# Kernel optimization log

Hardware: AMD Instinct MI355X
Metric: run time of the kernel (lower is better)

The kernel has to match this reference:

```python
import jax, jax.numpy as jnp
import numpy as np

EOS = 1          # endToken[0]
T = 50           # maxDecodingTime (hard-coded in module)
B, S = 64, 128   # batch, src_len
E_ENC = 1024     # enc_hidden_size (== dec_hidden_size, required by outNN)
H = 1024         # dec_hidden_size
EMB = 512        # embed_size
V = 32000        # output vocab


def setup_inputs() -> dict:
    key = jax.random.key(0)
    ks = jax.random.split(key, 10)
    def p(k, shape, fan_in):
        return jax.random.normal(k, shape, jnp.float32) / np.float32(np.sqrt(fan_in))
    return {
        'dec_initial_state': jax.random.normal(ks[0], (2, 1, B, H), jnp.float32),
        'enc_hiddens': jax.random.normal(ks[1], (B, S, E_ENC), jnp.float32),
        'enc_len': jax.random.randint(ks[2], (B,), 1, S + 1),
        'tgt': jax.random.randint(ks[3], (B, T), 0, V),  # unused in eval mode (training=False)
        'W_ih': p(ks[4], (4 * H, EMB), EMB),      # LSTM input weights (i,f,g,o)
        'W_hh': p(ks[5], (4 * H, H), H),          # LSTM hidden weights
        'b_lstm': jnp.zeros((4 * H,), jnp.float32),
        'W_attproj': p(ks[6], (H, E_ENC), E_ENC), # att_projection (no bias)
        'W_out': p(ks[7], (EMB, 2 * E_ENC), 2 * E_ENC),  # outNN (no bias)
        'W_vocab': p(ks[8], (V, EMB), EMB),       # vocab_projection (no bias)
        'emb_table': p(ks[9], (V, EMB), 1.0),     # seqEmb
    }


def reference(dec_initial_state, enc_hiddens, enc_len, tgt, W_ih, W_hh, b_lstm,
              W_attproj, W_out, W_vocab, emb_table):
    # eval mode: tgt unused, dropout is identity
    h0 = dec_initial_state[0, 0]  # [B,H]
    c0 = dec_initial_state[1, 0]  # [B,H]
    keys = jnp.einsum('bse,he->bsh', enc_hiddens, W_attproj)          # att keys [B,S,H]
    mask = jnp.arange(S)[None, :] < enc_len[:, None]                  # sent mask [B,S]
    NEG = jnp.float32(-1e9)
    prev0 = jnp.zeros((B, EMB), jnp.float32)
    tl0 = jnp.zeros((B,), jnp.int32)
    fl0 = jnp.zeros((B,), bool)

    def step(carry, t):
        h, c, prev, tl, fl = carry
        # LSTM cell
        gates = prev @ W_ih.T + h @ W_hh.T + b_lstm                   # [B,4H]
        i, f, g, o = jnp.split(gates, 4, axis=1)
        c = jax.nn.sigmoid(f) * c + jax.nn.sigmoid(i) * jnp.tanh(g)
        h = jax.nn.sigmoid(o) * jnp.tanh(c)
        # dot attention over encoder states
        scores = jnp.einsum('bsh,bh->bs', keys, h)
        alpha = jax.nn.softmax(jnp.where(mask, scores, NEG), axis=1)
        c_t = jnp.einsum('bs,bse->be', alpha, enc_hiddens)            # [B,E_ENC]
        dec = jnp.concatenate([h, c_t], axis=1) @ W_out.T             # [B,EMB]
        sym = jnp.argmax(dec @ W_vocab.T, axis=1)                     # greedy symbol
        prev = emb_table[sym]
        is_eos = sym == EOS
        tl = jnp.where(is_eos, t + 1, tl)
        fl = fl | is_eos
        return (h, c, prev, tl, fl), (dec, is_eos)

    (_, _, _, tl, _), (preds, eos_hist) = jax.lax.scan(
        step, (h0, c0, prev0, tl0, fl0), jnp.arange(T))
    tl = jnp.where(~eos_hist[-1], T, tl)       # torch: tgt_len[~ixEOS] = decoding_time
    preds = preds.transpose(1, 0, 2)           # [B,T,EMB]
    logP = jax.nn.log_softmax(preds @ W_vocab.T, axis=2)  # [B,T,V]
    return logP, tl
```

## Files before the change

kernel.cpp:

```cpp
#include <hip/hip_runtime.h>
#include <math.h>

#define BB  64
#define SS  128
#define HH  1024
#define EE  1024
#define EMBD 512
#define VV  32000
#define TT  50

#define OFF_H     0
#define OFF_C     65536
#define OFF_PREV  131072
#define OFF_HC    163840
#define OFF_GPART 294912
#define OFF_DPART 1867776
#define OFF_DEC   2129920
#define OFF_QPART 2162688
#define OFF_TVAL  2424832
#define OFF_TIDX  2456832
#define OFF_SYM   2488832
#define OFF_TL    2488896
#define OFF_KEYS  2488960
#define WS_NEED_KEYS ((size_t)(OFF_KEYS + 8388608) * 4)

template<bool BT>
__device__ __forceinline__ void gemm_tile(const float* __restrict__ A, int lda,
                                          const float* __restrict__ B, int ldb,
                                          float* __restrict__ C, size_t ldc, int K)
{
    __shared__ __attribute__((aligned(16))) float As[32][68];
    __shared__ __attribute__((aligned(16))) float Bs[32][68];
    int tid = threadIdx.x;
    int tx = tid & 15, ty = tid >> 4;
    float acc[4][4] = {};
    int lr = tid >> 2;
    int lk = (tid & 3) << 3;
    int bk = tid >> 3;
    int bn = (tid & 7) << 3;

    for (int kc = 0; kc < K; kc += 32) {
        float4 a0 = *(const float4*)(A + (size_t)lr * lda + kc + lk);
        float4 a1 = *(const float4*)(A + (size_t)lr * lda + kc + lk + 4);
        As[lk+0][lr] = a0.x; As[lk+1][lr] = a0.y; As[lk+2][lr] = a0.z; As[lk+3][lr] = a0.w;
        As[lk+4][lr] = a1.x; As[lk+5][lr] = a1.y; As[lk+6][lr] = a1.z; As[lk+7][lr] = a1.w;
        if (BT) {
            float4 b0 = *(const float4*)(B + (size_t)lr * ldb + kc + lk);
            float4 b1 = *(const float4*)(B + (size_t)lr * ldb + kc + lk + 4);
            Bs[lk+0][lr] = b0.x; Bs[lk+1][lr] = b0.y; Bs[lk+2][lr] = b0.z; Bs[lk+3][lr] = b0.w;
            Bs[lk+4][lr] = b1.x; Bs[lk+5][lr] = b1.y; Bs[lk+6][lr] = b1.z; Bs[lk+7][lr] = b1.w;
        } else {
            float4 b0 = *(const float4*)(B + (size_t)(kc + bk) * ldb + bn);
            float4 b1 = *(const float4*)(B + (size_t)(kc + bk) * ldb + bn + 4);
            *(float4*)&Bs[bk][bn]     = b0;
            *(float4*)&Bs[bk][bn + 4] = b1;
        }
        __syncthreads();
        #pragma unroll 8
        for (int k = 0; k < 32; ++k) {
            float4 av = *(const float4*)&As[k][ty << 2];
            float4 bv = *(const float4*)&Bs[k][tx << 2];
            float am[4] = {av.x, av.y, av.z, av.w};
            float bm[4] = {bv.x, bv.y, bv.z, bv.w};
            #pragma unroll
            for (int i = 0; i < 4; ++i)
                #pragma unroll
                for (int j = 0; j < 4; ++j)
                    acc[i][j] = fmaf(am[i], bm[j], acc[i][j]);
        }
        __syncthreads();
    }
    #pragma unroll
    for (int i = 0; i < 4; ++i) {
        float4 w = make_float4(acc[i][0], acc[i][1], acc[i][2], acc[i][3]);
        *(float4*)(C + (size_t)((ty << 2) + i) * ldc + (tx << 2)) = w;
    }
}

__global__ __launch_bounds__(256) void k_gemm_bt(const float* __restrict__ A, int lda,
                                                 const float* __restrict__ B, int ldb,
                                                 float* __restrict__ C, long long ldc,
                                                 int KC, long long partStride)
{
    int n0 = blockIdx.x << 6;
    int k0 = blockIdx.y * KC;
    gemm_tile<true>(A + k0, lda, B + (size_t)n0 * ldb + k0, ldb,
                    C + (size_t)blockIdx.y * partStride + n0, (size_t)ldc, KC);
}

__global__ __launch_bounds__(256) void k_gemm_bn(const float* __restrict__ A, int lda,
                                                 const float* __restrict__ B, int ldb,
                                                 float* __restrict__ C, long long ldc,
                                                 int KC, long long partStride)
{
    int n0 = blockIdx.x << 6;
    int k0 = blockIdx.y * KC;
    gemm_tile<false>(A + k0, lda, B + (size_t)k0 * ldb + n0, ldb,
                     C + (size_t)blockIdx.y * partStride + n0, (size_t)ldc, KC);
}

__global__ __launch_bounds__(256) void k_keys(const float* __restrict__ enc,
                                              const float* __restrict__ Wap,
                                              float* __restrict__ keys)
{
    int n0 = blockIdx.x << 6;
    int m0 = blockIdx.y << 6;
    gemm_tile<true>(enc + (size_t)m0 * EE, EE, Wap + (size_t)n0 * EE, EE,
                    keys + (size_t)m0 * HH + n0, (size_t)HH, EE);
}

__global__ __launch_bounds__(256) void k_gates(const float* __restrict__ prev,
                                               const float* __restrict__ h,
                                               const float* __restrict__ Wih,
                                               const float* __restrict__ Whh,
                                               float* __restrict__ part)
{
    int n0 = blockIdx.x << 6;
    int ks = blockIdx.y;
    const float* A; const float* Bp; int lda, ldb;
    if (ks < 2) { A = prev + ks * 256;      lda = EMBD; Bp = Wih + (size_t)n0 * EMBD + ks * 256;       ldb = EMBD; }
    else        { A = h + (ks - 2) * 256;   lda = HH;   Bp = Whh + (size_t)n0 * HH + (ks - 2) * 256;   ldb = HH;   }
    gemm_tile<true>(A, lda, Bp, ldb, part + (size_t)ks * 262144 + n0, 4096, 256);
}

__global__ void k_lstm(const float* __restrict__ part, const float* __restrict__ bias,
                       float* __restrict__ h, float* __restrict__ c, float* __restrict__ hc)
{
    int idx = blockIdx.x * 256 + threadIdx.x;
    int b = idx >> 10, j = idx & 1023;
    size_t base = (size_t)b * 4096;
    #define GATE(col) (part[base + (col)] + part[base + (col) + 262144] + part[base + (col) + 524288] \
                     + part[base + (col) + 786432] + part[base + (col) + 1048576] + part[base + (col) + 1310720] \
                     + bias[(col)])
    float gi = GATE(j);
    float gf = GATE(j + 1024);
    float gg = GATE(j + 2048);
    float go = GATE(j + 3072);
    #undef GATE
    float si = 1.f / (1.f + expf(-gi));
    float sf = 1.f / (1.f + expf(-gf));
    float so = 1.f / (1.f + expf(-go));
    float cn = sf * c[idx] + si * tanhf(gg);
    float hn = so * tanhf(cn);
    c[idx] = cn;
    h[idx] = hn;
    hc[(size_t)b * 2048 + j] = hn;
}

__global__ __launch_bounds__(1024) void k_attn(const float* __restrict__ keys,
                                               const float* __restrict__ enc,
                                               const int* __restrict__ enc_len,
                                               const float* __restrict__ h,
                                               float* __restrict__ hc)
{
    __shared__ float hs[1024];
    __shared__ float sc[128];
    __shared__ float4 red[3][256];
    int b = blockIdx.x, tid = threadIdx.x;
    hs[tid] = h[(size_t)b * 1024 + tid];
    __syncthreads();
    int lane = tid & 63, w = tid >> 6;
    const float* kb = keys + (size_t)b * SS * HH;
    for (int s = w; s < 128; s += 16) {
        const float* kr = kb + (size_t)s * 1024;
        float acc = 0.f;
        #pragma unroll
        for (int i = 0; i < 16; ++i) acc = fmaf(kr[i * 64 + lane], hs[i * 64 + lane], acc);
        #pragma unroll
        for (int off = 32; off; off >>= 1) acc += __shfl_xor(acc, off, 64);
        if (lane == 0) sc[s] = acc;
    }
    __syncthreads();
    int len = enc_len[b];
    if (tid < 64) {
        float a  = (tid < len)      ? sc[tid]      : -1e9f;
        float a2 = (tid + 64 < len) ? sc[tid + 64] : -1e9f;
        float m = fmaxf(a, a2);
        #pragma unroll
        for (int off = 32; off; off >>= 1) m = fmaxf(m, __shfl_xor(m, off, 64));
        float ea = expf(a - m), ea2 = expf(a2 - m);
        float ssum = ea + ea2;
        #pragma unroll
        for (int off = 32; off; off >>= 1) ssum += __shfl_xor(ssum, off, 64);
        sc[tid] = ea / ssum; sc[tid + 64] = ea2 / ssum;
    }
    __syncthreads();
    int g = tid >> 8, t2 = tid & 255;
    const float* eb = enc + (size_t)b * SS * EE;
    float4 a4 = make_float4(0.f, 0.f, 0.f, 0.f);
    for (int s = g * 32; s < g * 32 + 32; ++s) {
        float al = sc[s];
        float4 e = *(const float4*)(eb + (size_t)s * 1024 + t2 * 4);
        a4.x = fmaf(al, e.x, a4.x); a4.y = fmaf(al, e.y, a4.y);
        a4.z = fmaf(al, e.z, a4.z); a4.w = fmaf(al, e.w, a4.w);
    }
    if (g) red[g - 1][t2] = a4;
    __syncthreads();
    if (g == 0) {
        float4 r1 = red[0][t2], r2 = red[1][t2], r3 = red[2][t2];
        a4.x += r1.x + r2.x + r3.x; a4.y += r1.y + r2.y + r3.y;
        a4.z += r1.z + r2.z + r3.z; a4.w += r1.w + r2.w + r3.w;
        *(float4*)(hc + (size_t)b * 2048 + 1024 + t2 * 4) = a4;
    }
}

__global__ __launch_bounds__(256) void k_attn_fb(const float* __restrict__ qpart,
                                                 const float* __restrict__ enc,
                                                 const int* __restrict__ enc_len,
                                                 float* __restrict__ hc)
{
    __shared__ float qs[1024];
    __shared__ float sc[128];
    int b = blockIdx.x, tid = threadIdx.x;
    for (int e = tid; e < 1024; e += 256) {
        size_t o = (size_t)b * 1024 + e;
        qs[e] = qpart[o] + qpart[o + 65536] + qpart[o + 131072] + qpart[o + 196608];
    }
    __syncthreads();
    int lane = tid & 63, w = tid >> 6;
    const float* eb = enc + (size_t)b * SS * EE;
    for (int s = w; s < 128; s += 4) {
        const float* er = eb + (size_t)s * 1024;
        float acc = 0.f;
        #pragma unroll
        for (int i = 0; i < 16; ++i) acc = fmaf(er[i * 64 + lane], qs[i * 64 + lane], acc);
        #pragma unroll
        for (int off = 32; off; off >>= 1) acc += __shfl_xor(acc, off, 64);
        if (lane == 0) sc[s] = acc;
    }
    __syncthreads();
    int len = enc_len[b];
    if (tid < 64) {
        float a  = (tid < len)      ? sc[tid]      : -1e9f;
        float a2 = (tid + 64 < len) ? sc[tid + 64] : -1e9f;
        float m = fmaxf(a, a2);
        #pragma unroll
        for (int off = 32; off; off >>= 1) m = fmaxf(m, __shfl_xor(m, off, 64));
        float ea = expf(a - m), ea2 = expf(a2 - m);
        float ssum = ea + ea2;
        #pragma unroll
        for (int off = 32; off; off >>= 1) ssum += __shfl_xor(ssum, off, 64);
        sc[tid] = ea / ssum; sc[tid + 64] = ea2 / ssum;
    }
    __syncthreads();
    float acc[4] = {0.f, 0.f, 0.f, 0.f};
    for (int s = 0; s < 128; ++s) {
        float al = sc[s];
        const float* er = eb + (size_t)s * 1024;
        #pragma unroll
        for (int j = 0; j < 4; ++j) acc[j] = fmaf(al, er[tid + j * 256], acc[j]);
    }
    #pragma unroll
    for (int j = 0; j < 4; ++j) hc[(size_t)b * 2048 + 1024 + tid + j * 256] = acc[j];
}

__global__ void k_reduce_dec(const float* __restrict__ part, float* __restrict__ dec)
{
    int i = blockIdx.x * 256 + threadIdx.x;
    float s = 0.f;
    #pragma unroll
    for (int p = 0; p < 8; ++p) s += part[p * 32768 + i];
    dec[i] = s;
}

__global__ __launch_bounds__(256) void k_vocab(const float* __restrict__ A,
                                               const float* __restrict__ B,
                                               float* __restrict__ out, int t,
                                               float* __restrict__ tval, int* __restrict__ tidx)
{
    __shared__ __attribute__((aligned(16))) float As[32][68];
    __shared__ __attribute__((aligned(16))) float Bs[32][68];
    int n0 = blockIdx.x << 6;
    const float* Bp = B + (size_t)n0 * EMBD;
    int tid = threadIdx.x;
    int tx = tid & 15, ty = tid >> 4;
    float acc[4][4] = {};
    int lr = tid >> 2;
    int lk = (tid & 3) << 3;

    for (int kc = 0; kc < EMBD; kc += 32) {
        float4 a0 = *(const float4*)(A + (size_t)lr * EMBD + kc + lk);
        float4 a1 = *(const float4*)(A + (size_t)lr * EMBD + kc + lk + 4);
        As[lk+0][lr] = a0.x; As[lk+1][lr] = a0.y; As[lk+2][lr] = a0.z; As[lk+3][lr] = a0.w;
        As[lk+4][lr] = a1.x; As[lk+5][lr] = a1.y; As[lk+6][lr] = a1.z; As[lk+7][lr] = a1.w;
        float4 b0 = *(const float4*)(Bp + (size_t)lr * EMBD + kc + lk);
        float4 b1 = *(const float4*)(Bp + (size_t)lr * EMBD + kc + lk + 4);
        Bs[lk+0][lr] = b0.x; Bs[lk+1][lr] = b0.y; Bs[lk+2][lr] = b0.z; Bs[lk+3][lr] = b0.w;
        Bs[lk+4][lr] = b1.x; Bs[lk+5][lr] = b1.y; Bs[lk+6][lr] = b1.z; Bs[lk+7][lr] = b1.w;
        __syncthreads();
        #pragma unroll 8
        for (int k = 0; k < 32; ++k) {
            float4 av = *(const float4*)&As[k][ty << 2];
            float4 bv = *(const float4*)&Bs[k][tx << 2];
            float am[4] = {av.x, av.y, av.z, av.w};
            float bm[4] = {bv.x, bv.y, bv.z, bv.w};
            #pragma unroll
            for (int i = 0; i < 4; ++i)
                #pragma unroll
                for (int j = 0; j < 4; ++j)
                    acc[i][j] = fmaf(am[i], bm[j], acc[i][j]);
        }
        __syncthreads();
    }
    size_t ldc = (size_t)TT * VV;
    float* Cb = out + (size_t)t * VV + n0;
    #pragma unroll
    for (int i = 0; i < 4; ++i) {
        float4 w = make_float4(acc[i][0], acc[i][1], acc[i][2], acc[i][3]);
        *(float4*)(Cb + (size_t)((ty << 2) + i) * ldc + (tx << 2)) = w;
    }
    #pragma unroll
    for (int i = 0; i < 4; ++i) {
        float v = acc[i][0]; int jx = 0;
        if (acc[i][1] > v) { v = acc[i][1]; jx = 1; }
        if (acc[i][2] > v) { v = acc[i][2]; jx = 2; }
        if (acc[i][3] > v) { v = acc[i][3]; jx = 3; }
        int gi = n0 + (tx << 2) + jx;
        #pragma unroll
        for (int mk = 1; mk < 16; mk <<= 1) {
            float ov = __shfl_xor(v, mk, 64);
            int   oi = __shfl_xor(gi, mk, 64);
            if (ov > v || (ov == v && oi < gi)) { v = ov; gi = oi; }
        }
        if (tx == 0) {
            tval[blockIdx.x * 64 + (ty << 2) + i] = v;
            tidx[blockIdx.x * 64 + (ty << 2) + i] = gi;
        }
    }
}

__global__ __launch_bounds__(256) void k_argmax2(const float* __restrict__ tval,
                                                 const int* __restrict__ tidx,
                                                 const float* __restrict__ emb,
                                                 float* __restrict__ prev,
                                                 int* __restrict__ sym, int* __restrict__ tl, int t)
{
    __shared__ float bv[256];
    __shared__ int   bi[256];
    int b = blockIdx.x, tid = threadIdx.x;
    float mv = -INFINITY; int mi = 0x7fffffff;
    for (int tile = tid; tile < 500; tile += 256) {
        float v = tval[tile * 64 + b];
        int  ix = tidx[tile * 64 + b];
        if (v > mv || (v == mv && ix < mi)) { mv = v; mi = ix; }
    }
    bv[tid] = mv; bi[tid] = mi;
    __syncthreads();
    for (int s = 128; s; s >>= 1) {
        if (tid < s) {
            float ov = bv[tid + s]; int oi = bi[tid + s];
            if (ov > bv[tid] || (ov == bv[tid] && oi < bi[tid])) { bv[tid] = ov; bi[tid] = oi; }
        }
        __syncthreads();
    }
    int best = bi[0];
    if (tid == 0) { sym[b] = best; if (best == 1) tl[b] = t + 1; }
    for (int e = tid; e < 128; e += 256)
        ((float4*)(prev + (size_t)b * EMBD))[e] = ((const float4*)(emb + (size_t)best * EMBD))[e];
}

__global__ void k_tl(const int* __restrict__ sym, const int* __restrict__ tl, float* __restrict__ out_tl)
{
    int b = threadIdx.x;
    out_tl[b] = (float)((sym[b] == 1) ? tl[b] : TT);
}

__global__ __launch_bounds__(256) void k_logsm(float* __restrict__ out)
{
    __shared__ float rm[256], rs[256];
    size_t base = (size_t)blockIdx.x * VV;
    int tid = threadIdx.x;
    float m = -INFINITY, s = 0.f;
    for (int v = tid; v < VV; v += 256) {
        float x = out[base + v];
        if (x > m) { s = s * expf(m - x) + 1.f; m = x; }
        else       { s += expf(x - m); }
    }
    rm[tid] = m; rs[tid] = s;
    __syncthreads();
    for (int st = 128; st; st >>= 1) {
        if (tid < st) {
            float m2 = rm[tid + st], s2 = rs[tid + st];
            float M = fmaxf(rm[tid], m2);
            rs[tid] = rs[tid] * expf(rm[tid] - M) + s2 * expf(m2 - M);
            rm[tid] = M;
        }
        __syncthreads();
    }
    float lse = rm[0] + logf(rs[0]);
    for (int v = tid; v < VV; v += 256) out[base + v] -= lse;
}

__global__ void k_init(const float* __restrict__ dis, float* __restrict__ h, float* __restrict__ c,
                       float* __restrict__ prev, int* __restrict__ tl)
{
    int idx = blockIdx.x * 256 + threadIdx.x;
    h[idx] = dis[idx];
    c[idx] = dis[65536 + idx];
    if (idx < 32768) prev[idx] = 0.f;
    if (idx < 64) tl[idx] = 0;
}

extern "C" void kernel_launch(void* const* d_in, const int* in_sizes, int n_in,
                              void* d_out, int out_size, void* d_ws, size_t ws_size,
                              hipStream_t stream)
{
    const float* dis  = (const float*)d_in[0];
    const float* enc  = (const float*)d_in[1];
    const int*   elen = (const int*)  d_in[2];
    const float* Wih  = (const float*)d_in[4];
    const float* Whh  = (const float*)d_in[5];
    const float* bl   = (const float*)d_in[6];
    const float* Wap  = (const float*)d_in[7];
    const float* Wout = (const float*)d_in[8];
    const float* Wvoc = (const float*)d_in[9];
    const float* emb  = (const float*)d_in[10];
    float* out = (float*)d_out;
    float* ws  = (float*)d_ws;

    float* h     = ws + OFF_H;
    float* c     = ws + OFF_C;
    float* prev  = ws + OFF_PREV;
    float* hc    = ws + OFF_HC;
    float* gpart = ws + OFF_GPART;
    float* dpart = ws + OFF_DPART;
    float* dec   = ws + OFF_DEC;
    float* qpart = ws + OFF_QPART;
    float* tval  = ws + OFF_TVAL;
    int*   tidx  = (int*)(ws + OFF_TIDX);
    int*   sym   = (int*)(ws + OFF_SYM);
    int*   tl    = (int*)(ws + OFF_TL);
    float* keys  = ws + OFF_KEYS;

    const bool use_keys = ws_size >= WS_NEED_KEYS;

    k_init<<<256, 256, 0, stream>>>(dis, h, c, prev, tl);
    if (use_keys)
        k_keys<<<dim3(16, 128), 256, 0, stream>>>(enc, Wap, keys);

    for (int t = 0; t < TT; ++t) {
        k_gates<<<dim3(64, 6), 256, 0, stream>>>(prev, h, Wih, Whh, gpart);
        k_lstm<<<256, 256, 0, stream>>>(gpart, bl, h, c, hc);
        if (use_keys) {
            k_attn<<<64, 1024, 0, stream>>>(keys, enc, elen, h, hc);
        } else {
            k_gemm_bn<<<dim3(16, 4), 256, 0, stream>>>(h, HH, Wap, EE, qpart, EE, 256, 65536);
            k_attn_fb<<<64, 256, 0, stream>>>(qpart, enc, elen, hc);
        }
        k_gemm_bt<<<dim3(8, 8), 256, 0, stream>>>(hc, 2048, Wout, 2048, dpart, 512, 256, 32768);
        k_reduce_dec<<<128, 256, 0, stream>>>(dpart, dec);
        k_vocab<<<500, 256, 0, stream>>>(dec, Wvoc, out, t, tval, tidx);
        k_argmax2<<<64, 256, 0, stream>>>(tval, tidx, emb, prev, sym, tl, t);
    }

    k_tl<<<1, 64, 0, stream>>>(sym, tl, out + (size_t)BB * TT * VV);
    k_logsm<<<3200, 256, 0, stream>>>(out);
}
```

Measured before the change: 6.059 ms.

## Fuse LSTM into attention, compute online log-sum-exp in vocab GEMM, retile GEMMs

Several unrelated changes land together. The vocab GEMM now also computes per-tile exp-sums, so the log-sum-exp is finished in the argmax kernel and the final pass only subtracts it instead of re-reading every row twice. The LSTM cell update is merged into the attention kernel, which removes one launch per step. The keys and vocab GEMMs move to larger 128-wide tiles, while the gates and outNN GEMMs use more K-splits to get more blocks. The cost is larger partial-sum buffers and more reduction traffic, and the fused kernel runs on only 64 blocks.

```diff
diff --git a/kernel.cpp b/kernel.cpp
--- a/kernel.cpp
+++ b/kernel.cpp
@@ -8,20 +8,23 @@
 #define EMBD 512
 #define VV  32000
 #define TT  50
+#define NTILE 250
 
 #define OFF_H     0
 #define OFF_C     65536
 #define OFF_PREV  131072
 #define OFF_HC    163840
 #define OFF_GPART 294912
-#define OFF_DPART 1867776
-#define OFF_DEC   2129920
-#define OFF_QPART 2162688
-#define OFF_TVAL  2424832
-#define OFF_TIDX  2456832
-#define OFF_SYM   2488832
-#define OFF_TL    2488896
-#define OFF_KEYS  2488960
+#define OFF_DPART 3440640
+#define OFF_DEC   3964928
+#define OFF_QPART 3997696
+#define OFF_TVAL  4259840
+#define OFF_TIDX  4276224
+#define OFF_TSUM  4292608
+#define OFF_LSE   4308992
+#define OFF_SYM   4313088
+#define OFF_TL    4313152
+#define OFF_KEYS  4313216
 #define WS_NEED_KEYS ((size_t)(OFF_KEYS + 8388608) * 4)
 
 template<bool BT>
@@ -103,10 +106,58 @@
                                               const float* __restrict__ Wap,
                                               float* __restrict__ keys)
 {
-    int n0 = blockIdx.x << 6;
-    int m0 = blockIdx.y << 6;
-    gemm_tile<true>(enc + (size_t)m0 * EE, EE, Wap + (size_t)n0 * EE, EE,
-                    keys + (size_t)m0 * HH + n0, (size_t)HH, EE);
+    __shared__ __attribute__((aligned(16))) float As[32][136];
+    __shared__ __attribute__((aligned(16))) float Bs[32][136];
+    int n0 = blockIdx.x << 7;
+    int m0 = blockIdx.y << 7;
+    int tid = threadIdx.x;
+    int tx = tid & 15, ty = tid >> 4;
+    int lr = tid >> 1, lk = (tid & 1) << 4;
+    float acc[8][8] = {};
+    const float* Arow = enc + (size_t)(m0 + lr) * EE + lk;
+    const float* Brow = Wap + (size_t)(n0 + lr) * EE + lk;
+
+    for (int kc = 0; kc < EE; kc += 32) {
+        float4 a0 = *(const float4*)(Arow + kc);
+        float4 a1 = *(const float4*)(Arow + kc + 4);
+        float4 a2 = *(const float4*)(Arow + kc + 8);
+        float4 a3 = *(const float4*)(Arow + kc + 12);
+        As[lk+ 0][lr]=a0.x; As[lk+ 1][lr]=a0.y; As[lk+ 2][lr]=a0.z; As[lk+ 3][lr]=a0.w;
+        As[lk+ 4][lr]=a1.x; As[lk+ 5][lr]=a1.y; As[lk+ 6][lr]=a1.z; As[lk+ 7][lr]=a1.w;
+        As[lk+ 8][lr]=a2.x; As[lk+ 9][lr]=a2.y; As[lk+10][lr]=a2.z; As[lk+11][lr]=a2.w;
+        As[lk+12][lr]=a3.x; As[lk+13][lr]=a3.y; As[lk+14][lr]=a3.z; As[lk+15][lr]=a3.w;
+        float4 b0 = *(const float4*)(Brow + kc);
+        float4 b1 = *(const float4*)(Brow + kc + 4);
+        float4 b2 = *(const float4*)(Brow + kc + 8);
+        float4 b3 = *(const float4*)(Brow + kc + 12);
+        Bs[lk+ 0][lr]=b0.x; Bs[lk+ 1][lr]=b0.y; Bs[lk+ 2][lr]=b0.z; Bs[lk+ 3][lr]=b0.w;
+        Bs[lk+ 4][lr]=b1.x; Bs[lk+ 5][lr]=b1.y; Bs[lk+ 6][lr]=b1.z; Bs[lk+ 7][lr]=b1.w;
+        Bs[lk+ 8][lr]=b2.x; Bs[lk+ 9][lr]=b2.y; Bs[lk+10][lr]=b2.z; Bs[lk+11][lr]=b2.w;
+        Bs[lk+12][lr]=b3.x; Bs[lk+13][lr]=b3.y; Bs[lk+14][lr]=b3.z; Bs[lk+15][lr]=b3.w;
+        __syncthreads();
+        #pragma unroll 4
+        for (int k = 0; k < 32; ++k) {
+            float4 av0 = *(const float4*)&As[k][ty << 2];
+            float4 av1 = *(const float4*)&As[k][64 + (ty << 2)];
+            float4 bv0 = *(const float4*)&Bs[k][tx << 2];
+            float4 bv1 = *(const float4*)&Bs[k][64 + (tx << 2)];
+            float am[8] = {av0.x,av0.y,av0.z,av0.w, av1.x,av1.y,av1.z,av1.w};
+            float bm[8] = {bv0.x,bv0.y,bv0.z,bv0.w, bv1.x,bv1.y,bv1.z,bv1.w};
+            #pragma unroll
+            for (int i = 0; i < 8; ++i)
+                #pragma unroll
+                for (int j = 0; j < 8; ++j)
+                    acc[i][j] = fmaf(am[i], bm[j], acc[i][j]);
+        }
+        __syncthreads();
+    }
+    #pragma unroll
+    for (int i = 0; i < 8; ++i) {
+        int r = m0 + ((i < 4) ? (ty << 2) + i : 64 + (ty << 2) + (i - 4));
+        float* kr = keys + (size_t)r * HH + n0;
+        *(float4*)(kr + (tx << 2))      = make_float4(acc[i][0], acc[i][1], acc[i][2], acc[i][3]);
+        *(float4*)(kr + 64 + (tx << 2)) = make_float4(acc[i][4], acc[i][5], acc[i][6], acc[i][7]);
+    }
 }
 
 __global__ __launch_bounds__(256) void k_gates(const float* __restrict__ prev,
@@ -118,9 +169,87 @@
     int n0 = blockIdx.x << 6;
     int ks = blockIdx.y;
     const float* A; const float* Bp; int lda, ldb;
-    if (ks < 2) { A = prev + ks * 256;      lda = EMBD; Bp = Wih + (size_t)n0 * EMBD + ks * 256;       ldb = EMBD; }
-    else        { A = h + (ks - 2) * 256;   lda = HH;   Bp = Whh + (size_t)n0 * HH + (ks - 2) * 256;   ldb = HH;   }
-    gemm_tile<true>(A, lda, Bp, ldb, part + (size_t)ks * 262144 + n0, 4096, 256);
+    if (ks < 4) { A = prev + ks * 128;      lda = EMBD; Bp = Wih + (size_t)n0 * EMBD + ks * 128;       ldb = EMBD; }
+    else        { A = h + (ks - 4) * 128;   lda = HH;   Bp = Whh + (size_t)n0 * HH + (ks - 4) * 128;   ldb = HH;   }
+    gemm_tile<true>(A, lda, Bp, ldb, part + (size_t)ks * 262144 + n0, 4096, 128);
+}
+
+__global__ __launch_bounds__(1024) void k_lstm_attn(const float* __restrict__ part,
+                                                    const float* __restrict__ bias,
+                                                    const float* __restrict__ keys,
+                                                    const float* __restrict__ enc,
+                                                    const int* __restrict__ enc_len,
+                                                    float* __restrict__ h,
+                                                    float* __restrict__ c,
+                                                    float* __restrict__ hc)
+{
+    __shared__ float hs[1024];
+    __shared__ float sc[128];
+    __shared__ float4 red[3][256];
+    int b = blockIdx.x, tid = threadIdx.x;
+    {
+        size_t base = (size_t)b * 4096;
+        float gi = bias[tid], gf = bias[tid + 1024], gg = bias[tid + 2048], go = bias[tid + 3072];
+        #pragma unroll
+        for (int p = 0; p < 12; ++p) {
+            const float* pp = part + (size_t)p * 3145728 / 12 + base;
+            gi += pp[tid]; gf += pp[tid + 1024]; gg += pp[tid + 2048]; go += pp[tid + 3072];
+        }
+        float si = 1.f / (1.f + expf(-gi));
+        float sf = 1.f / (1.f + expf(-gf));
+        float so = 1.f / (1.f + expf(-go));
+        int idx = b * 1024 + tid;
+        float cn = sf * c[idx] + si * tanhf(gg);
+        float hn = so * tanhf(cn);
+        c[idx] = cn;
+        h[idx] = hn;
+        hc[(size_t)b * 2048 + tid] = hn;
+        hs[tid] = hn;
+    }
+    __syncthreads();
+    int lane = tid & 63, w = tid >> 6;
+    const float* kb = keys + (size_t)b * SS * HH;
+    for (int s = w; s < 128; s += 16) {
+        const float* kr = kb + (size_t)s * 1024;
+        float acc = 0.f;
+        #pragma unroll
+        for (int i = 0; i < 16; ++i) acc = fmaf(kr[i * 64 + lane], hs[i * 64 + lane], acc);
+        #pragma unroll
+        for (int off = 32; off; off >>= 1) acc += __shfl_xor(acc, off, 64);
+        if (lane == 0) sc[s] = acc;
+    }
+    __syncthreads();
+    int len = enc_len[b];
+    if (tid < 64) {
+        float a  = (tid < len)      ? sc[tid]      : -1e9f;
+        float a2 = (tid + 64 < len) ? sc[tid + 64] : -1e9f;
+        float m = fmaxf(a, a2);
+        #pragma unroll
+        for (int off = 32; off; off >>= 1) m = fmaxf(m, __shfl_xor(m, off, 64));
+        float ea = expf(a - m), ea2 = expf(a2 - m);
+        float ssum = ea + ea2;
+        #pragma unroll
+        for (int off = 32; off; off >>= 1) ssum += __shfl_xor(ssum, off, 64);
+        sc[tid] = ea / ssum; sc[tid + 64] = ea2 / ssum;
+    }
+    __syncthreads();
+    int g = tid >> 8, t2 = tid & 255;
+    const float* eb = enc + (size_t)b * SS * EE;
+    float4 a4 = make_float4(0.f, 0.f, 0.f, 0.f);
+    for (int s = g * 32; s < g * 32 + 32; ++s) {
+        float al = sc[s];
+        float4 e = *(const float4*)(eb + (size_t)s * 1024 + t2 * 4);
+        a4.x = fmaf(al, e.x, a4.x); a4.y = fmaf(al, e.y, a4.y);
+        a4.z = fmaf(al, e.z, a4.z); a4.w = fmaf(al, e.w, a4.w);
+    }
+    if (g) red[g - 1][t2] = a4;
+    __syncthreads();
+    if (g == 0) {
+        float4 r1 = red[0][t2], r2 = red[1][t2], r3 = red[2][t2];
+        a4.x += r1.x + r2.x + r3.x; a4.y += r1.y + r2.y + r3.y;
+        a4.z += r1.z + r2.z + r3.z; a4.w += r1.w + r2.w + r3.w;
+        *(float4*)(hc + (size_t)b * 2048 + 1024 + t2 * 4) = a4;
+    }
 }
 
 __global__ void k_lstm(const float* __restrict__ part, const float* __restrict__ bias,
@@ -129,14 +258,12 @@
     int idx = blockIdx.x * 256 + threadIdx.x;
     int b = idx >> 10, j = idx & 1023;
     size_t base = (size_t)b * 4096;
-    #define GATE(col) (part[base + (col)] + part[base + (col) + 262144] + part[base + (col) + 524288] \
-                     + part[base + (col) + 786432] + part[base + (col) + 1048576] + part[base + (col) + 1310720] \
-                     + bias[(col)])
-    float gi = GATE(j);
-    float gf = GATE(j + 1024);
-    float gg = GATE(j + 2048);
-    float go = GATE(j + 3072);
-    #undef GATE
+    float gi = bias[j], gf = bias[j + 1024], gg = bias[j + 2048], go = bias[j + 3072];
+    #pragma unroll
+    for (int p = 0; p < 12; ++p) {
+        const float* pp = part + (size_t)p * 262144 + base;
+        gi += pp[j]; gf += pp[j + 1024]; gg += pp[j + 2048]; go += pp[j + 3072];
+    }
     float si = 1.f / (1.f + expf(-gi));
     float sf = 1.f / (1.f + expf(-gf));
     float so = 1.f / (1.f + expf(-go));
@@ -147,63 +274,6 @@
     hc[(size_t)b * 2048 + j] = hn;
 }
 
-__global__ __launch_bounds__(1024) void k_attn(const float* __restrict__ keys,
-                                               const float* __restrict__ enc,
-                                               const int* __restrict__ enc_len,
-                                               const float* __restrict__ h,
-                                               float* __restrict__ hc)
-{
-    __shared__ float hs[1024];
-    __shared__ float sc[128];
-    __shared__ float4 red[3][256];
-    int b = blockIdx.x, tid = threadIdx.x;
-    hs[tid] = h[(size_t)b * 1024 + tid];
-    __syncthreads();
-    int lane = tid & 63, w = tid >> 6;
-    const float* kb = keys + (size_t)b * SS * HH;
-    for (int s = w; s < 128; s += 16) {
-        const float* kr = kb + (size_t)s * 1024;
-        float acc = 0.f;
-        #pragma unroll
-        for (int i = 0; i < 16; ++i) acc = fmaf(kr[i * 64 + lane], hs[i * 64 + lane], acc);
-        #pragma unroll
-        for (int off = 32; off; off >>= 1) acc += __shfl_xor(acc, off, 64);
-        if (lane == 0) sc[s] = acc;
-    }
-    __syncthreads();
-    int len = enc_len[b];
-    if (tid < 64) {
-        float a  = (tid < len)      ? sc[tid]      : -1e9f;
-        float a2 = (tid + 64 < len) ? sc[tid + 64] : -1e9f;
-        float m = fmaxf(a, a2);
-        #pragma unroll
-        for (int off = 32; off; off >>= 1) m = fmaxf(m, __shfl_xor(m, off, 64));
-        float ea = expf(a - m), ea2 = expf(a2 - m);
-        float ssum = ea + ea2;
-        #pragma unroll
-        for (int off = 32; off; off >>= 1) ssum += __shfl_xor(ssum, off, 64);
-        sc[tid] = ea / ssum; sc[tid + 64] = ea2 / ssum;
-    }
-    __syncthreads();
-    int g = tid >> 8, t2 = tid & 255;
-    const float* eb = enc + (size_t)b * SS * EE;
-    float4 a4 = make_float4(0.f, 0.f, 0.f, 0.f);
-    for (int s = g * 32; s < g * 32 + 32; ++s) {
-        float al = sc[s];
-        float4 e = *(const float4*)(eb + (size_t)s * 1024 + t2 * 4);
-        a4.x = fmaf(al, e.x, a4.x); a4.y = fmaf(al, e.y, a4.y);
-        a4.z = fmaf(al, e.z, a4.z); a4.w = fmaf(al, e.w, a4.w);
-    }
-    if (g) red[g - 1][t2] = a4;
-    __syncthreads();
-    if (g == 0) {
-        float4 r1 = red[0][t2], r2 = red[1][t2], r3 = red[2][t2];
-        a4.x += r1.x + r2.x + r3.x; a4.y += r1.y + r2.y + r3.y;
-        a4.z += r1.z + r2.z + r3.z; a4.w += r1.w + r2.w + r3.w;
-        *(float4*)(hc + (size_t)b * 2048 + 1024 + t2 * 4) = a4;
-    }
-}
-
 __global__ __launch_bounds__(256) void k_attn_fb(const float* __restrict__ qpart,
                                                  const float* __restrict__ enc,
                                                  const int* __restrict__ enc_len,
@@ -257,47 +327,57 @@
 __global__ void k_reduce_dec(const float* __restrict__ part, float* __restrict__ dec)
 {
     int i = blockIdx.x * 256 + threadIdx.x;
-    float s = 0.f;
-    #pragma unroll
-    for (int p = 0; p < 8; ++p) s += part[p * 32768 + i];
-    dec[i] = s;
+    float4 s = ((const float4*)part)[i];
+    #pragma unroll
+    for (int p = 1; p < 16; ++p) {
+        float4 v = ((const float4*)part)[p * 8192 + i];
+        s.x += v.x; s.y += v.y; s.z += v.z; s.w += v.w;
+    }
+    ((float4*)dec)[i] = s;
 }
 
 __global__ __launch_bounds__(256) void k_vocab(const float* __restrict__ A,
                                                const float* __restrict__ B,
                                                float* __restrict__ out, int t,
-                                               float* __restrict__ tval, int* __restrict__ tidx)
+                                               float* __restrict__ tval, int* __restrict__ tidx,
+                                               float* __restrict__ tsum)
 {
     __shared__ __attribute__((aligned(16))) float As[32][68];
-    __shared__ __attribute__((aligned(16))) float Bs[32][68];
-    int n0 = blockIdx.x << 6;
+    __shared__ __attribute__((aligned(16))) float Bs[32][136];
+    int n0 = blockIdx.x << 7;
     const float* Bp = B + (size_t)n0 * EMBD;
     int tid = threadIdx.x;
     int tx = tid & 15, ty = tid >> 4;
-    float acc[4][4] = {};
-    int lr = tid >> 2;
-    int lk = (tid & 3) << 3;
+    float acc[4][8] = {};
+    int ar = tid >> 2, ak = (tid & 3) << 3;
+    int br = tid >> 1, bk = (tid & 1) << 4;
 
     for (int kc = 0; kc < EMBD; kc += 32) {
-        float4 a0 = *(const float4*)(A + (size_t)lr * EMBD + kc + lk);
-        float4 a1 = *(const float4*)(A + (size_t)lr * EMBD + kc + lk + 4);
-        As[lk+0][lr] = a0.x; As[lk+1][lr] = a0.y; As[lk+2][lr] = a0.z; As[lk+3][lr] = a0.w;
-        As[lk+4][lr] = a1.x; As[lk+5][lr] = a1.y; As[lk+6][lr] = a1.z; As[lk+7][lr] = a1.w;
-        float4 b0 = *(const float4*)(Bp + (size_t)lr * EMBD + kc + lk);
-        float4 b1 = *(const float4*)(Bp + (size_t)lr * EMBD + kc + lk + 4);
-        Bs[lk+0][lr] = b0.x; Bs[lk+1][lr] = b0.y; Bs[lk+2][lr] = b0.z; Bs[lk+3][lr] = b0.w;
-        Bs[lk+4][lr] = b1.x; Bs[lk+5][lr] = b1.y; Bs[lk+6][lr] = b1.z; Bs[lk+7][lr] = b1.w;
+        float4 a0 = *(const float4*)(A + (size_t)ar * EMBD + kc + ak);
+        float4 a1 = *(const float4*)(A + (size_t)ar * EMBD + kc + ak + 4);
+        As[ak+0][ar]=a0.x; As[ak+1][ar]=a0.y; As[ak+2][ar]=a0.z; As[ak+3][ar]=a0.w;
+        As[ak+4][ar]=a1.x; As[ak+5][ar]=a1.y; As[ak+6][ar]=a1.z; As[ak+7][ar]=a1.w;
+        const float* Brow = Bp + (size_t)br * EMBD + kc + bk;
+        float4 b0 = *(const float4*)(Brow);
+        float4 b1 = *(const float4*)(Brow + 4);
+        float4 b2 = *(const float4*)(Brow + 8);
+        float4 b3 = *(const float4*)(Brow + 12);
+        Bs[bk+ 0][br]=b0.x; Bs[bk+ 1][br]=b0.y; Bs[bk+ 2][br]=b0.z; Bs[bk+ 3][br]=b0.w;
+        Bs[bk+ 4][br]=b1.x; Bs[bk+ 5][br]=b1.y; Bs[bk+ 6][br]=b1.z; Bs[bk+ 7][br]=b1.w;
+        Bs[bk+ 8][br]=b2.x; Bs[bk+ 9][br]=b2.y; Bs[bk+10][br]=b2.z; Bs[bk+11][br]=b2.w;
+        Bs[bk+12][br]=b3.x; Bs[bk+13][br]=b3.y; Bs[bk+14][br]=b3.z; Bs[bk+15][br]=b3.w;
         __syncthreads();
         #pragma unroll 8
         for (int k = 0; k < 32; ++k) {
-            float4 av = *(const float4*)&As[k][ty << 2];
-            float4 bv = *(const float4*)&Bs[k][tx << 2];
+            float4 av  = *(const float4*)&As[k][ty << 2];
+            float4 bv0 = *(const float4*)&Bs[k][tx << 2];
+            float4 bv1 = *(const float4*)&Bs[k][64 + (tx << 2)];
             float am[4] = {av.x, av.y, av.z, av.w};
-            float bm[4] = {bv.x, bv.y, bv.z, bv.w};
+            float bm[8] = {bv0.x,bv0.y,bv0.z,bv0.w, bv1.x,bv1.y,bv1.z,bv1.w};
             #pragma unroll
             for (int i = 0; i < 4; ++i)
                 #pragma unroll
-                for (int j = 0; j < 4; ++j)
+                for (int j = 0; j < 8; ++j)
                     acc[i][j] = fmaf(am[i], bm[j], acc[i][j]);
         }
         __syncthreads();
@@ -306,44 +386,50 @@
     float* Cb = out + (size_t)t * VV + n0;
     #pragma unroll
     for (int i = 0; i < 4; ++i) {
-        float4 w = make_float4(acc[i][0], acc[i][1], acc[i][2], acc[i][3]);
-        *(float4*)(Cb + (size_t)((ty << 2) + i) * ldc + (tx << 2)) = w;
+        float* Cr = Cb + (size_t)((ty << 2) + i) * ldc;
+        *(float4*)(Cr + (tx << 2))      = make_float4(acc[i][0], acc[i][1], acc[i][2], acc[i][3]);
+        *(float4*)(Cr + 64 + (tx << 2)) = make_float4(acc[i][4], acc[i][5], acc[i][6], acc[i][7]);
     }
     #pragma unroll
     for (int i = 0; i < 4; ++i) {
         float v = acc[i][0]; int jx = 0;
-        if (acc[i][1] > v) { v = acc[i][1]; jx = 1; }
-        if (acc[i][2] > v) { v = acc[i][2]; jx = 2; }
-        if (acc[i][3] > v) { v = acc[i][3]; jx = 3; }
-        int gi = n0 + (tx << 2) + jx;
+        #pragma unroll
+        for (int j = 1; j < 8; ++j) if (acc[i][j] > v) { v = acc[i][j]; jx = j; }
+        int gi = n0 + ((jx < 4) ? (tx << 2) + jx : 64 + (tx << 2) + (jx - 4));
         #pragma unroll
         for (int mk = 1; mk < 16; mk <<= 1) {
             float ov = __shfl_xor(v, mk, 64);
             int   oi = __shfl_xor(gi, mk, 64);
             if (ov > v || (ov == v && oi < gi)) { v = ov; gi = oi; }
         }
+        float s = 0.f;
+        #pragma unroll
+        for (int j = 0; j < 8; ++j) s += expf(acc[i][j] - v);
+        #pragma unroll
+        for (int mk = 1; mk < 16; mk <<= 1) s += __shfl_xor(s, mk, 64);
         if (tx == 0) {
-            tval[blockIdx.x * 64 + (ty << 2) + i] = v;
-            tidx[blockIdx.x * 64 + (ty << 2) + i] = gi;
+            int row = (ty << 2) + i;
+            tval[blockIdx.x * 64 + row] = v;
+            tidx[blockIdx.x * 64 + row] = gi;
+            tsum[blockIdx.x * 64 + row] = s;
         }
     }
 }
 
 __global__ __launch_bounds__(256) void k_argmax2(const float* __restrict__ tval,
                                                  const int* __restrict__ tidx,
+                                                 const float* __restrict__ tsum,
                                                  const float* __restrict__ emb,
                                                  float* __restrict__ prev,
-                                                 int* __restrict__ sym, int* __restrict__ tl, int t)
+                                                 int* __restrict__ sym, int* __restrict__ tl,
+                                                 float* __restrict__ lse, int t)
 {
     __shared__ float bv[256];
     __shared__ int   bi[256];
+    __shared__ float bs[256];
     int b = blockIdx.x, tid = threadIdx.x;
     float mv = -INFINITY; int mi = 0x7fffffff;
-    for (int tile = tid; tile < 500; tile += 256) {
-        float v = tval[tile * 64 + b];
-        int  ix = tidx[tile * 64 + b];
-        if (v > mv || (v == mv && ix < mi)) { mv = v; mi = ix; }
-    }
+    if (tid < NTILE) { mv = tval[tid * 64 + b]; mi = tidx[tid * 64 + b]; }
     bv[tid] = mv; bi[tid] = mi;
     __syncthreads();
     for (int s = 128; s; s >>= 1) {
@@ -353,8 +439,22 @@
         }
         __syncthreads();
     }
+    float M = bv[0];
     int best = bi[0];
-    if (tid == 0) { sym[b] = best; if (best == 1) tl[b] = t + 1; }
+    __syncthreads();
+    float ps = 0.f;
+    if (tid < NTILE) ps = tsum[tid * 64 + b] * expf(tval[tid * 64 + b] - M);
+    bs[tid] = ps;
+    __syncthreads();
+    for (int s = 128; s; s >>= 1) {
+        if (tid < s) bs[tid] += bs[tid + s];
+        __syncthreads();
+    }
+    if (tid == 0) {
+        sym[b] = best;
+        if (best == 1) tl[b] = t + 1;
+        lse[b * TT + t] = M + logf(bs[0]);
+    }
     for (int e = tid; e < 128; e += 256)
         ((float4*)(prev + (size_t)b * EMBD))[e] = ((const float4*)(emb + (size_t)best * EMBD))[e];
 }
@@ -365,30 +465,15 @@
     out_tl[b] = (float)((sym[b] == 1) ? tl[b] : TT);
 }
 
-__global__ __launch_bounds__(256) void k_logsm(float* __restrict__ out)
-{
-    __shared__ float rm[256], rs[256];
-    size_t base = (size_t)blockIdx.x * VV;
-    int tid = threadIdx.x;
-    float m = -INFINITY, s = 0.f;
-    for (int v = tid; v < VV; v += 256) {
-        float x = out[base + v];
-        if (x > m) { s = s * expf(m - x) + 1.f; m = x; }
-        else       { s += expf(x - m); }
-    }
-    rm[tid] = m; rs[tid] = s;
-    __syncthreads();
-    for (int st = 128; st; st >>= 1) {
-        if (tid < st) {
-            float m2 = rm[tid + st], s2 = rs[tid + st];
-            float M = fmaxf(rm[tid], m2);
-            rs[tid] = rs[tid] * expf(rm[tid] - M) + s2 * expf(m2 - M);
-            rm[tid] = M;
-        }
-        __syncthreads();
-    }
-    float lse = rm[0] + logf(rs[0]);
-    for (int v = tid; v < VV; v += 256) out[base + v] -= lse;
+__global__ __launch_bounds__(256) void k_logsm_sub(float* __restrict__ out, const float* __restrict__ lse)
+{
+    float l = lse[blockIdx.x];
+    float4* o4 = (float4*)(out + (size_t)blockIdx.x * VV);
+    for (int v = threadIdx.x; v < 8000; v += 256) {
+        float4 x = o4[v];
+        x.x -= l; x.y -= l; x.z -= l; x.w -= l;
+        o4[v] = x;
+    }
 }
 
 __global__ void k_init(const float* __restrict__ dis, float* __restrict__ h, float* __restrict__ c,
@@ -428,6 +513,8 @@
     float* qpart = ws + OFF_QPART;
     float* tval  = ws + OFF_TVAL;
     int*   tidx  = (int*)(ws + OFF_TIDX);
+    float* tsum  = ws + OFF_TSUM;
+    float* lse   = ws + OFF_LSE;
     int*   sym   = (int*)(ws + OFF_SYM);
     int*   tl    = (int*)(ws + OFF_TL);
     float* keys  = ws + OFF_KEYS;
@@ -436,23 +523,23 @@
 
     k_init<<<256, 256, 0, stream>>>(dis, h, c, prev, tl);
     if (use_keys)
-        k_keys<<<dim3(16, 128), 256, 0, stream>>>(enc, Wap, keys);
+        k_keys<<<dim3(8, 64), 256, 0, stream>>>(enc, Wap, keys);
 
     for (int t = 0; t < TT; ++t) {
-        k_gates<<<dim3(64, 6), 256, 0, stream>>>(prev, h, Wih, Whh, gpart);
-        k_lstm<<<256, 256, 0, stream>>>(gpart, bl, h, c, hc);
+        k_gates<<<dim3(64, 12), 256, 0, stream>>>(prev, h, Wih, Whh, gpart);
         if (use_keys) {
-            k_attn<<<64, 1024, 0, stream>>>(keys, enc, elen, h, hc);
+            k_lstm_attn<<<64, 1024, 0, stream>>>(gpart, bl, keys, enc, elen, h, c, hc);
         } else {
+            k_lstm<<<256, 256, 0, stream>>>(gpart, bl, h, c, hc);
             k_gemm_bn<<<dim3(16, 4), 256, 0, stream>>>(h, HH, Wap, EE, qpart, EE, 256, 65536);
             k_attn_fb<<<64, 256, 0, stream>>>(qpart, enc, elen, hc);
         }
-        k_gemm_bt<<<dim3(8, 8), 256, 0, stream>>>(hc, 2048, Wout, 2048, dpart, 512, 256, 32768);
-        k_reduce_dec<<<128, 256, 0, stream>>>(dpart, dec);
-        k_vocab<<<500, 256, 0, stream>>>(dec, Wvoc, out, t, tval, tidx);
-        k_argmax2<<<64, 256, 0, stream>>>(tval, tidx, emb, prev, sym, tl, t);
+        k_gemm_bt<<<dim3(8, 16), 256, 0, stream>>>(hc, 2048, Wout, 2048, dpart, 512, 128, 32768);
+        k_reduce_dec<<<32, 256, 0, stream>>>(dpart, dec);
+        k_vocab<<<NTILE, 256, 0, stream>>>(dec, Wvoc, out, t, tval, tidx, tsum);
+        k_argmax2<<<64, 256, 0, stream>>>(tval, tidx, tsum, emb, prev, sym, tl, lse, t);
     }
 
     k_tl<<<1, 64, 0, stream>>>(sym, tl, out + (size_t)BB * TT * VV);
-    k_logsm<<<3200, 256, 0, stream>>>(out);
-}
+    k_logsm_sub<<<3200, 256, 0, stream>>>(out, lse);
+}
```

New measurement: 5.712 ms. 5.7% less time.
